# Optimization experiments

Hardware: AMD Instinct MI355X
Metric: run time of the kernel (lower is better)

The kernel has to match this reference:

```python
import jax, jax.numpy as jnp
import numpy as np

H = 256  # hidden_units
B = 64   # batch
D = 2048 # question length


def setup_inputs() -> dict:
    key = jax.random.key(0)
    ks = jax.random.split(key, 9)
    s = 1.0 / np.sqrt(H)
    return {
        "context": jax.random.normal(ks[0], (B, H), dtype=jnp.float32),
        "question": jax.random.normal(ks[1], (B, D, H), dtype=jnp.float32),
        "hidden": jax.random.normal(ks[2], (1, B, H), dtype=jnp.float32),
        "W1": jax.random.uniform(ks[3], (H, H), jnp.float32, -s, s),  # linear_g1, no bias
        "W2": jax.random.uniform(ks[4], (H, H), jnp.float32, -s, s),  # linear_g2
        "b2": jax.random.uniform(ks[5], (H,), jnp.float32, -s, s),
        "W3": jax.random.uniform(ks[6], (H, H), jnp.float32, -s, s),  # linear_g3, no bias
        "W4": jax.random.uniform(ks[7], (1, H), jnp.float32, -s, s),  # linear_g4
        "b4": jax.random.uniform(ks[8], (1,), jnp.float32, -s, s),
    }


def reference(context, question, hidden, W1, W2, b2, W3, W4, b4):
    # hidden: (1,B,H) -> (B,1,H); linear_g3 (no bias)
    g3 = jnp.swapaxes(hidden, 0, 1) @ W3.T            # (B,1,H)
    # linear_g2 on context, then unsqueeze(1)
    g2 = (context @ W2.T + b2)[:, None, :]            # (B,1,H)
    # linear_g1 on question (no bias)
    g1 = question @ W1.T                              # (B,D,H)
    # The torch repeat/view sequence is exactly a broadcast add in (B,D,H)
    s = jnp.tanh(g2 + g3 + g1)                        # (B,D,H)
    scores = s @ W4.T + b4                            # (B,D,1)
    attn = jax.nn.softmax(scores, axis=1)             # softmax over D
    # attn.transpose(1,2) bmm question -> (B,1,H)
    return jnp.einsum('bdo,bdh->boh', attn, question)
```

## Files before the change

kernel.cpp:

```cpp
#include <hip/hip_runtime.h>
#include <hip/hip_bf16.h>
#include <math.h>

#define HD 256
#define BB 64
#define DD 2048
#define NQ 4
#define NST 8

typedef __attribute__((ext_vector_type(8))) short  short8;
typedef __attribute__((ext_vector_type(4))) float  float4v;
typedef __attribute__((ext_vector_type(4))) unsigned uint4v;
typedef __attribute__((ext_vector_type(4))) unsigned short ushort4v;

__device__ inline unsigned short f2bf(float f) {
    unsigned u = __builtin_bit_cast(unsigned, f);
    u += 0x7FFFu + ((u >> 16) & 1u);
    return (unsigned short)(u >> 16);
}

__device__ inline short8 cvt8(float4v lo, float4v hi) {
    uint4v u;
    asm("v_cvt_pk_bf16_f32 %0, %1, %2" : "=v"(u[0]) : "v"(lo[0]), "v"(lo[1]));
    asm("v_cvt_pk_bf16_f32 %0, %1, %2" : "=v"(u[1]) : "v"(lo[2]), "v"(lo[3]));
    asm("v_cvt_pk_bf16_f32 %0, %1, %2" : "=v"(u[2]) : "v"(hi[0]), "v"(hi[1]));
    asm("v_cvt_pk_bf16_f32 %0, %1, %2" : "=v"(u[3]) : "v"(hi[2]), "v"(hi[3]));
    return __builtin_bit_cast(short8, u);
}

__device__ inline float fast_exp2(float x) {
    float r;
    asm("v_exp_f32 %0, %1" : "=v"(r) : "v"(x));
    return r;
}
__device__ inline float fast_expf(float x) { return fast_exp2(x * 1.4426950408889634f); }
__device__ inline float fast_tanh(float x) {
    float y = x * 2.8853900817779268f;
    y = fminf(fmaxf(y, -30.f), 30.f);
    float t = fast_exp2(y);
    float r;
    asm("v_rcp_f32 %0, %1" : "=v"(r) : "v"(t + 1.f));
    return (t - 1.f) * r;
}

#define SYNC_LDS() do { asm volatile("s_waitcnt lgkmcnt(0)" ::: "memory"); \
                        __builtin_amdgcn_s_barrier(); \
                        asm volatile("" ::: "memory"); } while (0)
#define WAITV8()  asm volatile("s_waitcnt vmcnt(8)" ::: "memory")
#define WAITV0()  asm volatile("s_waitcnt vmcnt(0)" ::: "memory")
#define BARRIER() do { __builtin_amdgcn_s_barrier(); asm volatile("" ::: "memory"); } while (0)

__device__ inline void load_lds16(const void* g, void* l) {
    __builtin_amdgcn_global_load_lds(
        (const __attribute__((address_space(1))) void*)g,
        (__attribute__((address_space(3))) void*)l, 16, 0, 0);
}

__device__ inline void stage(const float* qtile, float* buf, int wave, int lane) {
    const int half = lane & 1;
    #pragma unroll
    for (int i = 0; i < 8; ++i) {
        int r = wave * 8 + i;
        int gsrc = ((((lane >> 1) ^ (r & 7)) << 1) | half) << 4;
        load_lds16((const char*)qtile + (size_t)r * 1024 + gsrc,
                   (char*)buf + r * 1024);
    }
}

__global__ __launch_bounds__(256) void k_prep(const float* __restrict__ W1,
                                              unsigned short* __restrict__ w1b,
                                              const float* __restrict__ ctx,
                                              const float* __restrict__ hid,
                                              const float* __restrict__ W2,
                                              const float* __restrict__ b2,
                                              const float* __restrict__ W3,
                                              float* __restrict__ g23) {
    if (blockIdx.x < 64) {
        int i = blockIdx.x * 256 + threadIdx.x;
        float4v v = ((const float4v*)W1)[i];
        ushort4v o;
        o[0] = f2bf(v[0]); o[1] = f2bf(v[1]); o[2] = f2bf(v[2]); o[3] = f2bf(v[3]);
        ((ushort4v*)w1b)[i] = o;
    } else {
        int b = blockIdx.x - 64, t = threadIdx.x;
        __shared__ float c[HD], hh[HD];
        c[t]  = ctx[b * HD + t];
        hh[t] = hid[b * HD + t];
        __syncthreads();
        const float4v* w2 = (const float4v*)(W2 + (size_t)t * HD);
        const float4v* w3 = (const float4v*)(W3 + (size_t)t * HD);
        float acc = b2[t];
        #pragma unroll 8
        for (int k = 0; k < 64; ++k) {
            float4v a = w2[k], d = w3[k];
            int k4 = k * 4;
            acc += c[k4] * a[0] + c[k4 + 1] * a[1] + c[k4 + 2] * a[2] + c[k4 + 3] * a[3];
            acc += hh[k4] * d[0] + hh[k4 + 1] * d[1] + hh[k4 + 2] * d[2] + hh[k4 + 3] * d[3];
        }
        g23[b * HD + t] = acc;
    }
}

__global__ __launch_bounds__(512) void k_fused(const float* __restrict__ q,
                                               const unsigned short* __restrict__ w1b,
                                               const float* __restrict__ g23,
                                               const float* __restrict__ W4,
                                               float* __restrict__ pl,
                                               float* __restrict__ pO) {
    __shared__ __attribute__((aligned(16))) float buf0[64 * HD];
    __shared__ __attribute__((aligned(16))) float buf1[64 * HD];
    __shared__ float sp[8][64];

    const int t = threadIdx.x;
    const int qtr = blockIdx.x, b = blockIdx.y;
    const int lane = t & 63, wave = t >> 6;
    const int l15 = lane & 15, lk = lane >> 4;
    const int hb = wave * 32;
    const int cq = lane & 7, ro = lane >> 3;

    const float* qq = q + ((size_t)b * DD + qtr * 512) * HD;

    stage(qq, buf0, wave, lane);

    short8 bfr[8][2];
    #pragma unroll
    for (int kb = 0; kb < 8; ++kb)
        #pragma unroll
        for (int nf = 0; nf < 2; ++nf)
            bfr[kb][nf] = *(const short8*)&w1b[(size_t)(hb + nf * 16 + l15) * HD + kb * 32 + lk * 8];

    float gv[2][4], wv[2][4];
    #pragma unroll
    for (int nf = 0; nf < 2; ++nf)
        #pragma unroll
        for (int r = 0; r < 4; ++r) {
            int h = hb + nf * 16 + lk * 4 + r;
            gv[nf][r] = g23[b * HD + h];
            wv[nf][r] = W4[h];
        }

    float l = 0.f;
    float4v O = {0.f, 0.f, 0.f, 0.f};
    float* cur = buf0;
    float* nxt = buf1;

    #pragma unroll 1
    for (int st = 0; st < NST; ++st) {
        SYNC_LDS();
        if (st + 1 < NST) {
            stage(qq + (size_t)(st + 1) * 64 * HD, nxt, wave, lane);
            WAITV8();
        } else {
            WAITV0();
        }
        BARRIER();

        #pragma unroll
        for (int mf = 0; mf < 4; ++mf) {
            float4v acc0 = {0.f, 0.f, 0.f, 0.f}, acc1 = {0.f, 0.f, 0.f, 0.f};
            const int d = mf * 16 + l15;
            const int dsw = d & 7;
            #pragma unroll
            for (int kb = 0; kb < 8; ++kb) {
                int g = kb * 4 + lk;
                int byte = d * 1024 + ((g ^ dsw) << 5);
                float4v lo = *(const float4v*)((const char*)cur + byte);
                float4v hi = *(const float4v*)((const char*)cur + byte + 16);
                short8 bq = cvt8(lo, hi);
                acc0 = __builtin_amdgcn_mfma_f32_16x16x32_bf16(bfr[kb][0], bq, acc0, 0, 0, 0);
                acc1 = __builtin_amdgcn_mfma_f32_16x16x32_bf16(bfr[kb][1], bq, acc1, 0, 0, 0);
            }
            float s = 0.f;
            #pragma unroll
            for (int r = 0; r < 4; ++r) s += fast_tanh(acc0[r] + gv[0][r]) * wv[0][r];
            #pragma unroll
            for (int r = 0; r < 4; ++r) s += fast_tanh(acc1[r] + gv[1][r]) * wv[1][r];
            s += __shfl_xor(s, 16, 64);
            s += __shfl_xor(s, 32, 64);
            if (lk == 0) sp[wave][mf * 16 + l15] = s;
        }
        SYNC_LDS();

        float sc = sp[0][lane] + sp[1][lane] + sp[2][lane] + sp[3][lane]
                 + sp[4][lane] + sp[5][lane] + sp[6][lane] + sp[7][lane];
        float w = fast_exp2(sc * 1.4426950408889634f);
        l += w;
        const int gq = wave * 4 + (cq >> 1);
        const int hoff = (cq & 1) << 4;
        #pragma unroll
        for (int i = 0; i < 8; ++i) {
            int d = ro * 8 + i;
            float wd = __shfl(w, d, 64);
            int byte = d * 1024 + ((gq ^ (d & 7)) << 5) + hoff;
            float4v v = *(const float4v*)((const char*)cur + byte);
            O += wd * v;
        }

        float* tmp = cur; cur = nxt; nxt = tmp;
    }

    #pragma unroll
    for (int j = 0; j < 4; ++j) {
        O[j] += __shfl_xor(O[j], 8, 64);
        O[j] += __shfl_xor(O[j], 16, 64);
        O[j] += __shfl_xor(O[j], 32, 64);
    }
    if (ro == 0)
        *(float4v*)&pO[((size_t)(b * NQ + qtr)) * HD + wave * 32 + cq * 4] = O;

    l += __shfl_xor(l, 1, 64);
    l += __shfl_xor(l, 2, 64);
    l += __shfl_xor(l, 4, 64);
    l += __shfl_xor(l, 8, 64);
    l += __shfl_xor(l, 16, 64);
    l += __shfl_xor(l, 32, 64);
    if (t == 0) pl[b * NQ + qtr] = l;
}

__global__ __launch_bounds__(256) void k_comb(const float* __restrict__ pl,
                                              const float* __restrict__ pO,
                                              float* __restrict__ out) {
    int b = blockIdx.x, t = threadIdx.x;
    float L = pl[b * NQ] + pl[b * NQ + 1] + pl[b * NQ + 2] + pl[b * NQ + 3];
    float s = 0.f;
    #pragma unroll
    for (int c = 0; c < NQ; ++c) s += pO[((size_t)(b * NQ + c)) * HD + t];
    out[b * HD + t] = s / L;
}

extern "C" void kernel_launch(void* const* d_in, const int* in_sizes, int n_in,
                              void* d_out, int out_size, void* d_ws, size_t ws_size,
                              hipStream_t stream) {
    (void)in_sizes; (void)n_in; (void)out_size; (void)ws_size;
    const float* ctx = (const float*)d_in[0];
    const float* q   = (const float*)d_in[1];
    const float* hid = (const float*)d_in[2];
    const float* W1  = (const float*)d_in[3];
    const float* W2  = (const float*)d_in[4];
    const float* b2  = (const float*)d_in[5];
    const float* W3  = (const float*)d_in[6];
    const float* W4  = (const float*)d_in[7];
    float* out = (float*)d_out;

    char* ws = (char*)d_ws;
    unsigned short* w1b = (unsigned short*)(ws);
    float* g23 = (float*)(ws + 131072);
    float* pl  = (float*)(ws + 196608);
    float* pO  = (float*)(ws + 197632);

    k_prep <<<dim3(128), dim3(256), 0, stream>>>(W1, w1b, ctx, hid, W2, b2, W3, g23);
    k_fused<<<dim3(NQ, BB), dim3(512), 0, stream>>>(q, w1b, g23, W4, pl, pO);
    k_comb <<<dim3(BB), dim3(256), 0, stream>>>(pl, pO, out);
}
```

Baseline: 68.21 us.

## Stage question tiles as bf16 in LDS via register prefetch, doubling chunks

Replaces the fp32 double-buffered LDS staging (direct global-to-LDS loads) with register prefetch of the next tile. Each tile is converted once to bf16 and written into a single swizzled LDS buffer. This cuts LDS use from 128KB to about 32KB per block, which allows more blocks per CU, and doubles the number of D chunks so the grid has 512 blocks. The g23 and W4 vectors now come from LDS. The attention-weighted sum reads bf16 question values, which lowers output precision.

```diff
diff --git a/kernel.cpp b/kernel.cpp
--- a/kernel.cpp
+++ b/kernel.cpp
@@ -5,8 +5,8 @@
 #define HD 256
 #define BB 64
 #define DD 2048
-#define NQ 4
-#define NST 8
+#define NCHK 8
+#define NST 4
 
 typedef __attribute__((ext_vector_type(8))) short  short8;
 typedef __attribute__((ext_vector_type(4))) float  float4v;
@@ -17,6 +17,9 @@
     unsigned u = __builtin_bit_cast(unsigned, f);
     u += 0x7FFFu + ((u >> 16) & 1u);
     return (unsigned short)(u >> 16);
+}
+__device__ inline float bf2f(unsigned short u) {
+    return __builtin_bit_cast(float, (unsigned)u << 16);
 }
 
 __device__ inline short8 cvt8(float4v lo, float4v hi) {
@@ -46,26 +49,6 @@
 #define SYNC_LDS() do { asm volatile("s_waitcnt lgkmcnt(0)" ::: "memory"); \
                         __builtin_amdgcn_s_barrier(); \
                         asm volatile("" ::: "memory"); } while (0)
-#define WAITV8()  asm volatile("s_waitcnt vmcnt(8)" ::: "memory")
-#define WAITV0()  asm volatile("s_waitcnt vmcnt(0)" ::: "memory")
-#define BARRIER() do { __builtin_amdgcn_s_barrier(); asm volatile("" ::: "memory"); } while (0)
-
-__device__ inline void load_lds16(const void* g, void* l) {
-    __builtin_amdgcn_global_load_lds(
-        (const __attribute__((address_space(1))) void*)g,
-        (__attribute__((address_space(3))) void*)l, 16, 0, 0);
-}
-
-__device__ inline void stage(const float* qtile, float* buf, int wave, int lane) {
-    const int half = lane & 1;
-    #pragma unroll
-    for (int i = 0; i < 8; ++i) {
-        int r = wave * 8 + i;
-        int gsrc = ((((lane >> 1) ^ (r & 7)) << 1) | half) << 4;
-        load_lds16((const char*)qtile + (size_t)r * 1024 + gsrc,
-                   (char*)buf + r * 1024);
-    }
-}
 
 __global__ __launch_bounds__(256) void k_prep(const float* __restrict__ W1,
                                               unsigned short* __restrict__ w1b,
@@ -107,20 +90,27 @@
                                                const float* __restrict__ W4,
                                                float* __restrict__ pl,
                                                float* __restrict__ pO) {
-    __shared__ __attribute__((aligned(16))) float buf0[64 * HD];
-    __shared__ __attribute__((aligned(16))) float buf1[64 * HD];
+    __shared__ __attribute__((aligned(16))) unsigned short tile[64 * HD];
     __shared__ float sp[8][64];
+    __shared__ float g23s[HD], w4s[HD];
 
     const int t = threadIdx.x;
-    const int qtr = blockIdx.x, b = blockIdx.y;
+    const int chunk = blockIdx.x, b = blockIdx.y;
     const int lane = t & 63, wave = t >> 6;
     const int l15 = lane & 15, lk = lane >> 4;
     const int hb = wave * 32;
-    const int cq = lane & 7, ro = lane >> 3;
-
-    const float* qq = q + ((size_t)b * DD + qtr * 512) * HD;
-
-    stage(qq, buf0, wave, lane);
+    const int cg = lane & 7, ro = lane >> 3;
+
+    const float* qc = q + ((size_t)b * DD + chunk * 256) * HD;
+
+    const int sr = t >> 3, scf = (t & 7) * 32;
+
+    float4v stg0, stg1, stg2, stg3, stg4, stg5, stg6, stg7;
+    {
+        const float4v* src = (const float4v*)(qc + (size_t)sr * HD + scf);
+        stg0 = src[0]; stg1 = src[1]; stg2 = src[2]; stg3 = src[3];
+        stg4 = src[4]; stg5 = src[5]; stg6 = src[6]; stg7 = src[7];
+    }
 
     short8 bfr[8][2];
     #pragma unroll
@@ -129,52 +119,62 @@
         for (int nf = 0; nf < 2; ++nf)
             bfr[kb][nf] = *(const short8*)&w1b[(size_t)(hb + nf * 16 + l15) * HD + kb * 32 + lk * 8];
 
-    float gv[2][4], wv[2][4];
-    #pragma unroll
-    for (int nf = 0; nf < 2; ++nf)
-        #pragma unroll
-        for (int r = 0; r < 4; ++r) {
-            int h = hb + nf * 16 + lk * 4 + r;
-            gv[nf][r] = g23[b * HD + h];
-            wv[nf][r] = W4[h];
-        }
+    if (t < 256) g23s[t] = g23[b * HD + t];
+    else         w4s[t - 256] = W4[t - 256];
 
     float l = 0.f;
     float4v O = {0.f, 0.f, 0.f, 0.f};
-    float* cur = buf0;
-    float* nxt = buf1;
 
     #pragma unroll 1
-    for (int st = 0; st < NST; ++st) {
+    for (int ts = 0; ts < NST; ++ts) {
         SYNC_LDS();
-        if (st + 1 < NST) {
-            stage(qq + (size_t)(st + 1) * 64 * HD, nxt, wave, lane);
-            WAITV8();
-        } else {
-            WAITV0();
-        }
-        BARRIER();
+
+        {
+            short8 p0 = cvt8(stg0, stg1);
+            short8 p1 = cvt8(stg2, stg3);
+            short8 p2 = cvt8(stg4, stg5);
+            short8 p3 = cvt8(stg6, stg7);
+            int base = sr * 512 + (t & 7) * 64;
+            int sw = (sr & 7) << 4;
+            *(short8*)((char*)tile + ((base)      ^ sw)) = p0;
+            *(short8*)((char*)tile + ((base + 16) ^ sw)) = p1;
+            *(short8*)((char*)tile + ((base + 32) ^ sw)) = p2;
+            *(short8*)((char*)tile + ((base + 48) ^ sw)) = p3;
+        }
+        if (ts + 1 < NST) {
+            const float4v* src = (const float4v*)(qc + (size_t)((ts + 1) * 64 + sr) * HD + scf);
+            stg0 = src[0]; stg1 = src[1]; stg2 = src[2]; stg3 = src[3];
+            stg4 = src[4]; stg5 = src[5]; stg6 = src[6]; stg7 = src[7];
+        }
+        SYNC_LDS();
 
         #pragma unroll
         for (int mf = 0; mf < 4; ++mf) {
             float4v acc0 = {0.f, 0.f, 0.f, 0.f}, acc1 = {0.f, 0.f, 0.f, 0.f};
             const int d = mf * 16 + l15;
-            const int dsw = d & 7;
+            const int dsw = (d & 7) << 4;
             #pragma unroll
             for (int kb = 0; kb < 8; ++kb) {
-                int g = kb * 4 + lk;
-                int byte = d * 1024 + ((g ^ dsw) << 5);
-                float4v lo = *(const float4v*)((const char*)cur + byte);
-                float4v hi = *(const float4v*)((const char*)cur + byte + 16);
-                short8 bq = cvt8(lo, hi);
+                int byte = d * 512 + kb * 64 + lk * 16;
+                short8 bq = *(const short8*)((const char*)tile + (byte ^ dsw));
                 acc0 = __builtin_amdgcn_mfma_f32_16x16x32_bf16(bfr[kb][0], bq, acc0, 0, 0, 0);
                 acc1 = __builtin_amdgcn_mfma_f32_16x16x32_bf16(bfr[kb][1], bq, acc1, 0, 0, 0);
             }
             float s = 0.f;
-            #pragma unroll
-            for (int r = 0; r < 4; ++r) s += fast_tanh(acc0[r] + gv[0][r]) * wv[0][r];
-            #pragma unroll
-            for (int r = 0; r < 4; ++r) s += fast_tanh(acc1[r] + gv[1][r]) * wv[1][r];
+            {
+                int h0 = hb + lk * 4;
+                float4v g4 = *(const float4v*)&g23s[h0];
+                float4v w4 = *(const float4v*)&w4s[h0];
+                #pragma unroll
+                for (int r = 0; r < 4; ++r) s += fast_tanh(acc0[r] + g4[r]) * w4[r];
+            }
+            {
+                int h0 = hb + 16 + lk * 4;
+                float4v g4 = *(const float4v*)&g23s[h0];
+                float4v w4 = *(const float4v*)&w4s[h0];
+                #pragma unroll
+                for (int r = 0; r < 4; ++r) s += fast_tanh(acc1[r] + g4[r]) * w4[r];
+            }
             s += __shfl_xor(s, 16, 64);
             s += __shfl_xor(s, 32, 64);
             if (lk == 0) sp[wave][mf * 16 + l15] = s;
@@ -185,18 +185,18 @@
                  + sp[4][lane] + sp[5][lane] + sp[6][lane] + sp[7][lane];
         float w = fast_exp2(sc * 1.4426950408889634f);
         l += w;
-        const int gq = wave * 4 + (cq >> 1);
-        const int hoff = (cq & 1) << 4;
+        const int cb = wave * 64 + cg * 8;
         #pragma unroll
         for (int i = 0; i < 8; ++i) {
             int d = ro * 8 + i;
             float wd = __shfl(w, d, 64);
-            int byte = d * 1024 + ((gq ^ (d & 7)) << 5) + hoff;
-            float4v v = *(const float4v*)((const char*)cur + byte);
-            O += wd * v;
-        }
-
-        float* tmp = cur; cur = nxt; nxt = tmp;
+            int byte = (d * 512 + cb) ^ ((d & 7) << 4);
+            ushort4v v = *(const ushort4v*)((const char*)tile + byte);
+            O[0] += wd * bf2f(v[0]);
+            O[1] += wd * bf2f(v[1]);
+            O[2] += wd * bf2f(v[2]);
+            O[3] += wd * bf2f(v[3]);
+        }
     }
 
     #pragma unroll
@@ -206,7 +206,7 @@
         O[j] += __shfl_xor(O[j], 32, 64);
     }
     if (ro == 0)
-        *(float4v*)&pO[((size_t)(b * NQ + qtr)) * HD + wave * 32 + cq * 4] = O;
+        *(float4v*)&pO[((size_t)(b * NCHK + chunk)) * HD + wave * 32 + cg * 4] = O;
 
     l += __shfl_xor(l, 1, 64);
     l += __shfl_xor(l, 2, 64);
@@ -214,17 +214,19 @@
     l += __shfl_xor(l, 8, 64);
     l += __shfl_xor(l, 16, 64);
     l += __shfl_xor(l, 32, 64);
-    if (t == 0) pl[b * NQ + qtr] = l;
+    if (t == 0) pl[b * NCHK + chunk] = l;
 }
 
 __global__ __launch_bounds__(256) void k_comb(const float* __restrict__ pl,
                                               const float* __restrict__ pO,
                                               float* __restrict__ out) {
     int b = blockIdx.x, t = threadIdx.x;
-    float L = pl[b * NQ] + pl[b * NQ + 1] + pl[b * NQ + 2] + pl[b * NQ + 3];
+    float L = 0.f;
+    #pragma unroll
+    for (int c = 0; c < NCHK; ++c) L += pl[b * NCHK + c];
     float s = 0.f;
     #pragma unroll
-    for (int c = 0; c < NQ; ++c) s += pO[((size_t)(b * NQ + c)) * HD + t];
+    for (int c = 0; c < NCHK; ++c) s += pO[((size_t)(b * NCHK + c)) * HD + t];
     out[b * HD + t] = s / L;
 }
 
@@ -246,9 +248,9 @@
     unsigned short* w1b = (unsigned short*)(ws);
     float* g23 = (float*)(ws + 131072);
     float* pl  = (float*)(ws + 196608);
-    float* pO  = (float*)(ws + 197632);
+    float* pO  = (float*)(ws + 198656);
 
     k_prep <<<dim3(128), dim3(256), 0, stream>>>(W1, w1b, ctx, hid, W2, b2, W3, g23);
-    k_fused<<<dim3(NQ, BB), dim3(512), 0, stream>>>(q, w1b, g23, W4, pl, pO);
+    k_fused<<<dim3(NCHK, BB), dim3(512), 0, stream>>>(q, w1b, g23, W4, pl, pO);
     k_comb <<<dim3(BB), dim3(256), 0, stream>>>(pl, pO, out);
 }
```

Result: slower. 73.81 us (+8.2%).
